# Kernel tuning notes

Hardware: AMD Instinct MI355X
Metric: run time of the kernel (lower is better)

## Reference

```python
import jax, jax.numpy as jnp
import numpy as np

T, B = 512, 2048
IN, E, H = 12, 15, 20


def setup_inputs() -> dict:
    key = jax.random.key(0)
    ks = jax.random.split(key, 9)
    def rnd(k, shape, scale):
        return jax.random.normal(k, shape, dtype=jnp.float32) * scale
    return {
        "marker_detections": rnd(ks[0], (T, B, IN), 1.0),
        "W_emb": rnd(ks[1], (E, IN), 1.0 / np.sqrt(IN)),
        "b_emb": rnd(ks[2], (E,), 0.1),
        "W_ih": rnd(ks[3], (4 * H, E), 1.0 / np.sqrt(H)),
        "b_ih": rnd(ks[4], (4 * H,), 0.1),
        "W_hh": rnd(ks[5], (4 * H, H), 1.0 / np.sqrt(H)),
        "b_hh": rnd(ks[6], (4 * H,), 0.1),
        "W_out": rnd(ks[7], (3, H), 1.0 / np.sqrt(H)),
        "b_out": rnd(ks[8], (3,), 0.1),
    }


def _lstm(x_gates, W_hh, b_hh, hidden_dim):
    # x_gates: (T, B, 4H) precomputed input projections (PyTorch gate order i,f,g,o)
    Bsz = x_gates.shape[1]
    h0 = jnp.zeros((Bsz, hidden_dim), x_gates.dtype)
    c0 = jnp.zeros((Bsz, hidden_dim), x_gates.dtype)

    def step(carry, xg):
        h, c = carry
        gates = xg + h @ W_hh.T + b_hh  # (B, 4H)
        i, f, g, o = jnp.split(gates, 4, axis=-1)
        i = jax.nn.sigmoid(i)
        f = jax.nn.sigmoid(f)
        g = jnp.tanh(g)
        o = jax.nn.sigmoid(o)
        c = f * c + i * g
        h = o * jnp.tanh(c)
        return (h, c), h

    _, hs = jax.lax.scan(step, (h0, c0), x_gates)
    return hs  # (T, B, H)


def reference(marker_detections, W_emb, b_emb, W_ih, b_ih, W_hh, b_hh, W_out, b_out):
    # embeddings: (T, B, E)
    emb = marker_detections @ W_emb.T + b_emb
    # precompute input-to-gate projections for all timesteps: (T, B, 4H)
    x_gates = emb @ W_ih.T + b_ih
    hs = _lstm(x_gates, W_hh, b_hh, H)  # (T, B, H)
    pos_space = hs @ W_out.T + b_out  # (T, B, 3)
    return pos_space
```

## Files before the change

### kernel.cpp

```cpp
#include <hip/hip_runtime.h>

#define T_STEPS 512
#define BATCH   2048
#define IN_F    12
#define E_F     15
#define H_F     20
#define G4      80
#define TC      32
#define NCHUNK  (T_STEPS / TC)

typedef float v2f __attribute__((ext_vector_type(2)));

#define OFF_MD   0
#define OFF_H    768
#define OFF_WC   (768 + 48)
#define OFF_BC   (OFF_WC + 960)
#define OFF_RAW  (OFF_BC + 80)
#define RAW_WEMB 0
#define RAW_WIH  180
#define RAW_BEMB 1380
#define RAW_BIH  1395
#define RAW_BHH  1475
#define SMEM_FLOATS (OFF_RAW + 1555)

#define PIN1(a)          asm volatile("" : "+v"(a))
#define PIN2(a,b)        asm volatile("" : "+v"(a), "+v"(b))
#define PIN4(a,b,c,d)    asm volatile("" : "+v"(a), "+v"(b), "+v"(c), "+v"(d))

__device__ __forceinline__ float fsig(float x) {
    float e = __builtin_amdgcn_exp2f(x * -1.442695040888963f);
    return __builtin_amdgcn_rcpf(1.0f + e);
}
__device__ __forceinline__ float ftanh(float x) {
    float e = __builtin_amdgcn_exp2f(x * -2.885390081777927f);
    return fmaf(2.0f, __builtin_amdgcn_rcpf(1.0f + e), -1.0f);
}
__device__ __forceinline__ v2f pkfma(v2f a, v2f b, v2f c) {
    return __builtin_elementwise_fma(a, b, c);
}

__global__ __launch_bounds__(64, 1) void lstm_tracker_kernel(
    const float* __restrict__ md,
    const float* __restrict__ W_emb, const float* __restrict__ b_emb,
    const float* __restrict__ W_ih,  const float* __restrict__ b_ih,
    const float* __restrict__ W_hh,  const float* __restrict__ b_hh,
    const float* __restrict__ W_out, const float* __restrict__ b_out,
    float* __restrict__ out)
{
    __shared__ __align__(16) float smem[SMEM_FLOATS];
    const int lane = threadIdx.x;
    const int bl   = lane >> 5;
    const int j    = lane & 31;
    const int jj   = (j < H_F) ? j : 0;
    const int b    = blockIdx.x * 2 + bl;

    float* raw = smem + OFF_RAW;
    for (int i = lane; i < E_F * IN_F; i += 64) raw[RAW_WEMB + i] = W_emb[i];
    for (int i = lane; i < G4 * E_F;  i += 64) raw[RAW_WIH  + i] = W_ih[i];
    if (lane < E_F) raw[RAW_BEMB + lane] = b_emb[lane];
    for (int g = lane; g < G4; g += 64) raw[RAW_BIH + g] = b_ih[g];
    for (int g = lane; g < G4; g += 64) raw[RAW_BHH + g] = b_hh[g];

    for (int idx = lane; idx < G4 * IN_F; idx += 64) {
        int g = idx / IN_F, c = idx - g * IN_F;
        float s = 0.f;
        #pragma unroll
        for (int e = 0; e < E_F; ++e)
            s += raw[RAW_WIH + g * E_F + e] * raw[RAW_WEMB + e * IN_F + c];
        smem[OFF_WC + idx] = s;
    }
    for (int g = lane; g < G4; g += 64) {
        float s = raw[RAW_BIH + g] + raw[RAW_BHH + g];
        #pragma unroll
        for (int e = 0; e < E_F; ++e)
            s += raw[RAW_WIH + g * E_F + e] * raw[RAW_BEMB + e];
        smem[OFF_BC + g] = s;
    }

    v2f wcI[6], wcF[6], wcG[6], wcO[6];
    #pragma unroll
    for (int k = 0; k < 6; ++k) {
        wcI[k] = *(const v2f*)(smem + OFF_WC + (jj           ) * IN_F + 2 * k);
        wcF[k] = *(const v2f*)(smem + OFF_WC + (jj +     H_F ) * IN_F + 2 * k);
        wcG[k] = *(const v2f*)(smem + OFF_WC + (jj + 2 * H_F ) * IN_F + 2 * k);
        wcO[k] = *(const v2f*)(smem + OFF_WC + (jj + 3 * H_F ) * IN_F + 2 * k);
    }
    float bcI = smem[OFF_BC + jj];
    float bcF = smem[OFF_BC + jj + H_F];
    float bcG = smem[OFF_BC + jj + 2 * H_F];
    float bcO = smem[OFF_BC + jj + 3 * H_F];

    v2f whI[10], whF[10], whG[10], whO[10];
    #pragma unroll
    for (int k = 0; k < 10; ++k) {
        whI[k] = *(const v2f*)(W_hh + (jj           ) * H_F + 2 * k);
        whF[k] = *(const v2f*)(W_hh + (jj +     H_F ) * H_F + 2 * k);
        whG[k] = *(const v2f*)(W_hh + (jj + 2 * H_F ) * H_F + 2 * k);
        whO[k] = *(const v2f*)(W_hh + (jj + 3 * H_F ) * H_F + 2 * k);
    }
    const int rr = (j < 3) ? j : 0;
    v2f wo[10];
    #pragma unroll
    for (int k = 0; k < 10; ++k) wo[k] = *(const v2f*)(W_out + rr * H_F + 2 * k);
    float bo = b_out[rr];

    v2f h2[10];
    #pragma unroll
    for (int k = 0; k < 10; ++k) h2[k] = (v2f){0.f, 0.f};
    float cc = 0.f;

    #pragma unroll 1
    for (int ch = 0; ch < NCHUNK; ++ch) {
        #pragma unroll
        for (int k = 0; k < 6; ++k) { PIN4(wcI[k], wcF[k], wcG[k], wcO[k]); }
        #pragma unroll
        for (int k = 0; k < 10; ++k) { PIN4(whI[k], whF[k], whG[k], whO[k]); PIN1(wo[k]); }
        PIN4(bcI, bcF, bcG, bcO); PIN1(bo);

        for (int idx = lane; idx < TC * 6; idx += 64) {
            int tt = idx / 6, w = idx - tt * 6;
            const float* src = md + ((size_t)(ch * TC + tt) * BATCH + (size_t)blockIdx.x * 2) * IN_F + w * 4;
            *(float4*)(smem + OFF_MD + tt * 24 + w * 4) = *(const float4*)src;
        }

        const float4* mr0 = (const float4*)(smem + OFF_MD + bl * IN_F);
        float4 m0 = mr0[0], m1 = mr0[1], m2 = mr0[2];

        #pragma unroll 1
        for (int tt = 0; tt < TC; ++tt) {
            v2f mm0 = {m0.x, m0.y}, mm1 = {m0.z, m0.w}, mm2 = {m1.x, m1.y};
            v2f mm3 = {m1.z, m1.w}, mm4 = {m2.x, m2.y}, mm5 = {m2.z, m2.w};
            v2f aI = pkfma(wcI[0], mm0, pkfma(wcI[1], mm1, pkfma(wcI[2], mm2,
                     pkfma(wcI[3], mm3, pkfma(wcI[4], mm4, pkfma(wcI[5], mm5, (v2f){bcI, 0.f}))))));
            v2f aF = pkfma(wcF[0], mm0, pkfma(wcF[1], mm1, pkfma(wcF[2], mm2,
                     pkfma(wcF[3], mm3, pkfma(wcF[4], mm4, pkfma(wcF[5], mm5, (v2f){bcF, 0.f}))))));
            v2f aG = pkfma(wcG[0], mm0, pkfma(wcG[1], mm1, pkfma(wcG[2], mm2,
                     pkfma(wcG[3], mm3, pkfma(wcG[4], mm4, pkfma(wcG[5], mm5, (v2f){bcG, 0.f}))))));
            v2f aO = pkfma(wcO[0], mm0, pkfma(wcO[1], mm1, pkfma(wcO[2], mm2,
                     pkfma(wcO[3], mm3, pkfma(wcO[4], mm4, pkfma(wcO[5], mm5, (v2f){bcO, 0.f}))))));

            if (tt + 1 < TC) {
                const float4* mn = (const float4*)(smem + OFF_MD + (tt + 1) * 24 + bl * IN_F);
                m0 = mn[0]; m1 = mn[1]; m2 = mn[2];
            }

            const int st = ch * TC + tt;
            v2f pa = pkfma(wo[0], h2[0], pkfma(wo[1], h2[1], pkfma(wo[2], h2[2],
                     pkfma(wo[3], h2[3], pkfma(wo[4], h2[4], pkfma(wo[5], h2[5],
                     pkfma(wo[6], h2[6], pkfma(wo[7], h2[7], pkfma(wo[8], h2[8],
                     wo[9] * h2[9])))))))));
            if (j < 3 && st > 0)
                out[((size_t)(st - 1) * BATCH + b) * 3 + j] = pa.x + pa.y + bo;

            v2f rI = pkfma(whI[0], h2[0], pkfma(whI[1], h2[1], pkfma(whI[2], h2[2],
                     pkfma(whI[3], h2[3], pkfma(whI[4], h2[4], pkfma(whI[5], h2[5],
                     pkfma(whI[6], h2[6], pkfma(whI[7], h2[7], pkfma(whI[8], h2[8],
                     whI[9] * h2[9])))))))));
            v2f rF = pkfma(whF[0], h2[0], pkfma(whF[1], h2[1], pkfma(whF[2], h2[2],
                     pkfma(whF[3], h2[3], pkfma(whF[4], h2[4], pkfma(whF[5], h2[5],
                     pkfma(whF[6], h2[6], pkfma(whF[7], h2[7], pkfma(whF[8], h2[8],
                     whF[9] * h2[9])))))))));
            v2f rG = pkfma(whG[0], h2[0], pkfma(whG[1], h2[1], pkfma(whG[2], h2[2],
                     pkfma(whG[3], h2[3], pkfma(whG[4], h2[4], pkfma(whG[5], h2[5],
                     pkfma(whG[6], h2[6], pkfma(whG[7], h2[7], pkfma(whG[8], h2[8],
                     whG[9] * h2[9])))))))));
            v2f rO = pkfma(whO[0], h2[0], pkfma(whO[1], h2[1], pkfma(whO[2], h2[2],
                     pkfma(whO[3], h2[3], pkfma(whO[4], h2[4], pkfma(whO[5], h2[5],
                     pkfma(whO[6], h2[6], pkfma(whO[7], h2[7], pkfma(whO[8], h2[8],
                     whO[9] * h2[9])))))))));

            v2f sI = aI + rI, sF = aF + rF, sG = aG + rG, sO = aO + rO;
            float ai = sI.x + sI.y;
            float af = sF.x + sF.y;
            float ag = sG.x + sG.y;
            float ao = sO.x + sO.y;

            float gi = fsig(ai);
            float gf = fsig(af);
            float gt = ftanh(ag);
            float go = fsig(ao);
            cc = fmaf(gf, cc, gi * gt);
            float hown = go * ftanh(cc);

            if (j < H_F) smem[OFF_H + bl * 24 + jj] = hown;
            const float4* hr = (const float4*)(smem + OFF_H + bl * 24);
            float4 h0 = hr[0], h1 = hr[1], hx = hr[2], h3 = hr[3], h4 = hr[4];
            h2[0] = (v2f){h0.x, h0.y}; h2[1] = (v2f){h0.z, h0.w};
            h2[2] = (v2f){h1.x, h1.y}; h2[3] = (v2f){h1.z, h1.w};
            h2[4] = (v2f){hx.x, hx.y}; h2[5] = (v2f){hx.z, hx.w};
            h2[6] = (v2f){h3.x, h3.y}; h2[7] = (v2f){h3.z, h3.w};
            h2[8] = (v2f){h4.x, h4.y}; h2[9] = (v2f){h4.z, h4.w};
        }
    }

    v2f pa = pkfma(wo[0], h2[0], pkfma(wo[1], h2[1], pkfma(wo[2], h2[2],
             pkfma(wo[3], h2[3], pkfma(wo[4], h2[4], pkfma(wo[5], h2[5],
             pkfma(wo[6], h2[6], pkfma(wo[7], h2[7], pkfma(wo[8], h2[8],
             wo[9] * h2[9])))))))));
    if (j < 3)
        out[((size_t)(T_STEPS - 1) * BATCH + b) * 3 + j] = pa.x + pa.y + bo;
}

extern "C" void kernel_launch(void* const* d_in, const int* in_sizes, int n_in,
                              void* d_out, int out_size, void* d_ws, size_t ws_size,
                              hipStream_t stream) {
    const float* md    = (const float*)d_in[0];
    const float* W_emb = (const float*)d_in[1];
    const float* b_emb = (const float*)d_in[2];
    const float* W_ih  = (const float*)d_in[3];
    const float* b_ih  = (const float*)d_in[4];
    const float* W_hh  = (const float*)d_in[5];
    const float* b_hh  = (const float*)d_in[6];
    const float* W_out = (const float*)d_in[7];
    const float* b_out = (const float*)d_in[8];
    float* out = (float*)d_out;

    hipLaunchKernelGGL(lstm_tracker_kernel, dim3(BATCH / 2), dim3(64), 0, stream,
                       md, W_emb, b_emb, W_ih, b_ih, W_hh, b_hh, W_out, b_out, out);
}
```

Before: 299.5 us.

## Defer output projection to per-chunk pass and split recurrent dot chains

Each step's hidden state now goes to its own slot in a per-chunk shared-memory history buffer instead of being overwritten in place. The 3-wide output projection is removed from the serial time loop and computed once per chunk from that buffer, using W_out and b_out staged in shared memory. The recurrent gate dot products are split into two independent half-chains to shorten dependency latency. The asm register pins are dropped and the launch-bounds attribute changes to waves_per_eu, which may alter register allocation. The cost is more shared memory and an extra loop over each chunk.

```diff
diff --git a/kernel.cpp b/kernel.cpp
--- a/kernel.cpp
+++ b/kernel.cpp
@@ -12,10 +12,11 @@
 typedef float v2f __attribute__((ext_vector_type(2)));
 
 #define OFF_MD   0
-#define OFF_H    768
-#define OFF_WC   (768 + 48)
+#define OFF_HH   768
+#define OFF_WC   (768 + 1536)
 #define OFF_BC   (OFF_WC + 960)
-#define OFF_RAW  (OFF_BC + 80)
+#define OFF_WO   (OFF_BC + 80)
+#define OFF_RAW  (OFF_WO + 80)
 #define RAW_WEMB 0
 #define RAW_WIH  180
 #define RAW_BEMB 1380
@@ -23,10 +24,6 @@
 #define RAW_BHH  1475
 #define SMEM_FLOATS (OFF_RAW + 1555)
 
-#define PIN1(a)          asm volatile("" : "+v"(a))
-#define PIN2(a,b)        asm volatile("" : "+v"(a), "+v"(b))
-#define PIN4(a,b,c,d)    asm volatile("" : "+v"(a), "+v"(b), "+v"(c), "+v"(d))
-
 __device__ __forceinline__ float fsig(float x) {
     float e = __builtin_amdgcn_exp2f(x * -1.442695040888963f);
     return __builtin_amdgcn_rcpf(1.0f + e);
@@ -39,7 +36,9 @@
     return __builtin_elementwise_fma(a, b, c);
 }
 
-__global__ __launch_bounds__(64, 1) void lstm_tracker_kernel(
+__global__ void __launch_bounds__(64)
+__attribute__((amdgpu_waves_per_eu(1, 1)))
+lstm_tracker_kernel(
     const float* __restrict__ md,
     const float* __restrict__ W_emb, const float* __restrict__ b_emb,
     const float* __restrict__ W_ih,  const float* __restrict__ b_ih,
@@ -52,7 +51,7 @@
     const int bl   = lane >> 5;
     const int j    = lane & 31;
     const int jj   = (j < H_F) ? j : 0;
-    const int b    = blockIdx.x * 2 + bl;
+    const size_t bbase = (size_t)blockIdx.x * 2;
 
     float* raw = smem + OFF_RAW;
     for (int i = lane; i < E_F * IN_F; i += 64) raw[RAW_WEMB + i] = W_emb[i];
@@ -60,6 +59,11 @@
     if (lane < E_F) raw[RAW_BEMB + lane] = b_emb[lane];
     for (int g = lane; g < G4; g += 64) raw[RAW_BIH + g] = b_ih[g];
     for (int g = lane; g < G4; g += 64) raw[RAW_BHH + g] = b_hh[g];
+    for (int i = lane; i < 3 * H_F; i += 64) {
+        int r = i / H_F, k = i - r * H_F;
+        smem[OFF_WO + r * 24 + k] = W_out[i];
+    }
+    if (lane < 3) smem[OFF_WO + 72 + lane] = b_out[lane];
 
     for (int idx = lane; idx < G4 * IN_F; idx += 64) {
         int g = idx / IN_F, c = idx - g * IN_F;
@@ -85,10 +89,10 @@
         wcG[k] = *(const v2f*)(smem + OFF_WC + (jj + 2 * H_F ) * IN_F + 2 * k);
         wcO[k] = *(const v2f*)(smem + OFF_WC + (jj + 3 * H_F ) * IN_F + 2 * k);
     }
-    float bcI = smem[OFF_BC + jj];
-    float bcF = smem[OFF_BC + jj + H_F];
-    float bcG = smem[OFF_BC + jj + 2 * H_F];
-    float bcO = smem[OFF_BC + jj + 3 * H_F];
+    const float bcI = smem[OFF_BC + jj];
+    const float bcF = smem[OFF_BC + jj + H_F];
+    const float bcG = smem[OFF_BC + jj + 2 * H_F];
+    const float bcO = smem[OFF_BC + jj + 3 * H_F];
 
     v2f whI[10], whF[10], whG[10], whO[10];
     #pragma unroll
@@ -98,11 +102,6 @@
         whG[k] = *(const v2f*)(W_hh + (jj + 2 * H_F ) * H_F + 2 * k);
         whO[k] = *(const v2f*)(W_hh + (jj + 3 * H_F ) * H_F + 2 * k);
     }
-    const int rr = (j < 3) ? j : 0;
-    v2f wo[10];
-    #pragma unroll
-    for (int k = 0; k < 10; ++k) wo[k] = *(const v2f*)(W_out + rr * H_F + 2 * k);
-    float bo = b_out[rr];
 
     v2f h2[10];
     #pragma unroll
@@ -111,15 +110,9 @@
 
     #pragma unroll 1
     for (int ch = 0; ch < NCHUNK; ++ch) {
-        #pragma unroll
-        for (int k = 0; k < 6; ++k) { PIN4(wcI[k], wcF[k], wcG[k], wcO[k]); }
-        #pragma unroll
-        for (int k = 0; k < 10; ++k) { PIN4(whI[k], whF[k], whG[k], whO[k]); PIN1(wo[k]); }
-        PIN4(bcI, bcF, bcG, bcO); PIN1(bo);
-
         for (int idx = lane; idx < TC * 6; idx += 64) {
             int tt = idx / 6, w = idx - tt * 6;
-            const float* src = md + ((size_t)(ch * TC + tt) * BATCH + (size_t)blockIdx.x * 2) * IN_F + w * 4;
+            const float* src = md + ((size_t)(ch * TC + tt) * BATCH + bbase) * IN_F + w * 4;
             *(float4*)(smem + OFF_MD + tt * 24 + w * 4) = *(const float4*)src;
         }
 
@@ -144,32 +137,27 @@
                 m0 = mn[0]; m1 = mn[1]; m2 = mn[2];
             }
 
-            const int st = ch * TC + tt;
-            v2f pa = pkfma(wo[0], h2[0], pkfma(wo[1], h2[1], pkfma(wo[2], h2[2],
-                     pkfma(wo[3], h2[3], pkfma(wo[4], h2[4], pkfma(wo[5], h2[5],
-                     pkfma(wo[6], h2[6], pkfma(wo[7], h2[7], pkfma(wo[8], h2[8],
-                     wo[9] * h2[9])))))))));
-            if (j < 3 && st > 0)
-                out[((size_t)(st - 1) * BATCH + b) * 3 + j] = pa.x + pa.y + bo;
-
-            v2f rI = pkfma(whI[0], h2[0], pkfma(whI[1], h2[1], pkfma(whI[2], h2[2],
-                     pkfma(whI[3], h2[3], pkfma(whI[4], h2[4], pkfma(whI[5], h2[5],
-                     pkfma(whI[6], h2[6], pkfma(whI[7], h2[7], pkfma(whI[8], h2[8],
-                     whI[9] * h2[9])))))))));
-            v2f rF = pkfma(whF[0], h2[0], pkfma(whF[1], h2[1], pkfma(whF[2], h2[2],
-                     pkfma(whF[3], h2[3], pkfma(whF[4], h2[4], pkfma(whF[5], h2[5],
-                     pkfma(whF[6], h2[6], pkfma(whF[7], h2[7], pkfma(whF[8], h2[8],
-                     whF[9] * h2[9])))))))));
-            v2f rG = pkfma(whG[0], h2[0], pkfma(whG[1], h2[1], pkfma(whG[2], h2[2],
-                     pkfma(whG[3], h2[3], pkfma(whG[4], h2[4], pkfma(whG[5], h2[5],
-                     pkfma(whG[6], h2[6], pkfma(whG[7], h2[7], pkfma(whG[8], h2[8],
-                     whG[9] * h2[9])))))))));
-            v2f rO = pkfma(whO[0], h2[0], pkfma(whO[1], h2[1], pkfma(whO[2], h2[2],
-                     pkfma(whO[3], h2[3], pkfma(whO[4], h2[4], pkfma(whO[5], h2[5],
-                     pkfma(whO[6], h2[6], pkfma(whO[7], h2[7], pkfma(whO[8], h2[8],
-                     whO[9] * h2[9])))))))));
-
-            v2f sI = aI + rI, sF = aF + rF, sG = aG + rG, sO = aO + rO;
+            v2f rIa = pkfma(whI[0], h2[0], pkfma(whI[1], h2[1], pkfma(whI[2], h2[2],
+                      pkfma(whI[3], h2[3], whI[4] * h2[4]))));
+            v2f rIb = pkfma(whI[5], h2[5], pkfma(whI[6], h2[6], pkfma(whI[7], h2[7],
+                      pkfma(whI[8], h2[8], whI[9] * h2[9]))));
+            v2f rFa = pkfma(whF[0], h2[0], pkfma(whF[1], h2[1], pkfma(whF[2], h2[2],
+                      pkfma(whF[3], h2[3], whF[4] * h2[4]))));
+            v2f rFb = pkfma(whF[5], h2[5], pkfma(whF[6], h2[6], pkfma(whF[7], h2[7],
+                      pkfma(whF[8], h2[8], whF[9] * h2[9]))));
+            v2f rGa = pkfma(whG[0], h2[0], pkfma(whG[1], h2[1], pkfma(whG[2], h2[2],
+                      pkfma(whG[3], h2[3], whG[4] * h2[4]))));
+            v2f rGb = pkfma(whG[5], h2[5], pkfma(whG[6], h2[6], pkfma(whG[7], h2[7],
+                      pkfma(whG[8], h2[8], whG[9] * h2[9]))));
+            v2f rOa = pkfma(whO[0], h2[0], pkfma(whO[1], h2[1], pkfma(whO[2], h2[2],
+                      pkfma(whO[3], h2[3], whO[4] * h2[4]))));
+            v2f rOb = pkfma(whO[5], h2[5], pkfma(whO[6], h2[6], pkfma(whO[7], h2[7],
+                      pkfma(whO[8], h2[8], whO[9] * h2[9]))));
+
+            v2f sI = aI + rIa + rIb;
+            v2f sF = aF + rFa + rFb;
+            v2f sG = aG + rGa + rGb;
+            v2f sO = aO + rOa + rOb;
             float ai = sI.x + sI.y;
             float af = sF.x + sF.y;
             float ag = sG.x + sG.y;
@@ -182,8 +170,9 @@
             cc = fmaf(gf, cc, gi * gt);
             float hown = go * ftanh(cc);
 
-            if (j < H_F) smem[OFF_H + bl * 24 + jj] = hown;
-            const float4* hr = (const float4*)(smem + OFF_H + bl * 24);
+            float* hslot = smem + OFF_HH + tt * 48 + bl * 24;
+            if (j < H_F) hslot[jj] = hown;
+            const float4* hr = (const float4*)hslot;
             float4 h0 = hr[0], h1 = hr[1], hx = hr[2], h3 = hr[3], h4 = hr[4];
             h2[0] = (v2f){h0.x, h0.y}; h2[1] = (v2f){h0.z, h0.w};
             h2[2] = (v2f){h1.x, h1.y}; h2[3] = (v2f){h1.z, h1.w};
@@ -191,14 +180,21 @@
             h2[6] = (v2f){h3.x, h3.y}; h2[7] = (v2f){h3.z, h3.w};
             h2[8] = (v2f){h4.x, h4.y}; h2[9] = (v2f){h4.z, h4.w};
         }
-    }
-
-    v2f pa = pkfma(wo[0], h2[0], pkfma(wo[1], h2[1], pkfma(wo[2], h2[2],
-             pkfma(wo[3], h2[3], pkfma(wo[4], h2[4], pkfma(wo[5], h2[5],
-             pkfma(wo[6], h2[6], pkfma(wo[7], h2[7], pkfma(wo[8], h2[8],
-             wo[9] * h2[9])))))))));
-    if (j < 3)
-        out[((size_t)(T_STEPS - 1) * BATCH + b) * 3 + j] = pa.x + pa.y + bo;
+
+        for (int idx = lane; idx < TC * 6; idx += 64) {
+            int tt = idx / 6, rem = idx - tt * 6;
+            int bb = rem / 3, r = rem - bb * 3;
+            const float4* hp = (const float4*)(smem + OFF_HH + tt * 48 + bb * 24);
+            const float4* wp = (const float4*)(smem + OFF_WO + r * 24);
+            float s = smem[OFF_WO + 72 + r];
+            #pragma unroll
+            for (int k = 0; k < 5; ++k) {
+                float4 hv = hp[k], wv = wp[k];
+                s += hv.x * wv.x + hv.y * wv.y + hv.z * wv.z + hv.w * wv.w;
+            }
+            out[((size_t)(ch * TC + tt) * BATCH + bbase + bb) * 3 + r] = s;
+        }
+    }
 }
 
 extern "C" void kernel_launch(void* const* d_in, const int* in_sizes, int n_in,
```

New measurement: 281.8 us. 1.06x faster.
